# Optimization experiments

Hardware: AMD Instinct MI355X
Metric: run time of the kernel (lower is better)

Reference implementation:

```python
import jax, jax.numpy as jnp
import numpy as np

# ---------------- static model configuration (mirrors NeuroNN.__init__) -------------
N = 2000
RATIO = 0.8
N_E = int(N * RATIO)
N_I = N - N_E
NMAX = 60          # Euler fixed-point steps (Nmax in Euler2fixedpt)
NAVG = 15          # trailing steps averaged for convergence metric (Navg)
DT = 1e-3
XTOL = 1e-5
XMIN = 1.0
V_THR = 20.0       # spike threshold of Ricciardi transfer fn (V_rest = 0)
SCALING_G = 1.0
W_FF = 30.0
SIG_EXT = 5.0
DEG = jnp.pi / 180.0

_IS_I = jnp.arange(N) >= N_E
PREF = jnp.concatenate([jnp.linspace(0.0, 179.99, N_E), jnp.linspace(0.0, 179.99, N_I)])
T_INV = 1.0 / jnp.where(_IS_I, 0.01 * 0.5, 0.01)          # T_E=0.01, T_I=0.005
TAU = jnp.where(_IS_I, 0.01, 0.01)                          # tau_E = tau_I = 0.01
TAU_REF = jnp.where(_IS_I, 0.001, 0.005)                    # refractory periods
# connection-type gather index: conn[i,j] = 2*(j is I) + (i is I)  -> 0:ee 1:ei 2:ie 3:ii
CONN = 2 * _IS_I[None, :].astype(jnp.int32) + _IS_I[:, None].astype(jnp.int32)
SIGN_COL = jnp.where(_IS_I, -1.0, 1.0)                      # Dale's law: sign by presynaptic column
DIFF = jnp.abs(PREF[:, None] - PREF[None, :])               # |pref_i - pref_j| (deg)

ORIENTATIONS = jnp.arange(12.0) * 15.0                       # [12]
CONTRASTS = jnp.array([0.0, 0.0432773, 0.103411, 0.186966, 0.303066, 0.464386, 0.68854, 1.0])
# circular Gaussian feed-forward drive, [12, N]
_gauss = jnp.exp((jnp.cos(2.0 * DEG * (ORIENTATIONS[:, None] - PREF[None, :])) - 1.0)
                 / (4.0 * (DEG * W_FF) ** 2))
# all 96 conditions flattened: index c*12 + o, shape [96, N]
INPUT_MEAN = (CONTRASTS[:, None, None] * 20.0 * SCALING_G * _gauss[None]).reshape(96, N)

# ------------- Ricciardi transfer function Phi (Sanzeni rational approximation) ------
_A = [0.22757881388024176, 0.77373949685442023, 0.32056016125642045,
      0.32171431660633076, 0.62718906618071668, 0.93524391761244940,
      1.0616084849547165, 0.64290613877355551, 0.14805913578876898]

def f_ricci(x):
    t = -x / (1.0 + x)
    p = jnp.zeros_like(x)
    for c in reversed(_A):      # Horner: a1*t + ... + a9*t^9
        p = p * t + c
    return jnp.log(2.0 * x + 1.0) + p * t

def g_ricci(x):
    z = x / (2.0 + x)
    enum = (3.5441754117462949 * z - 7.0529131065835378 * z**2 - 56.532378057580381 * z**3
            + 279.56761105465944 * z**4 - 520.37554793489681 * z**5
            + 456.58245777026514 * z**6 - 155.73340457809226 * z**7)
    denom = (1.0 - 4.1357968834226053 * z - 7.2984226138266743 * z**2
             + 98.656602235468327 * z**3 - 334.20436223415163 * z**4
             + 601.08633903294185 * z**5 - 599.58577549598340 * z**6
             + 277.18420330693891 * z**7 - 16.445022798669722 * z**8)
    return enum / denom

def Phi(mu, sigma, tau, tau_ref):
    xp = mu / sigma
    xm = (mu - V_THR) / sigma
    pos = xm > 0
    neg = xp <= 0
    mid = (~pos) & (~neg)
    # branch 1: 0 < xm < xp   (guard values keep unselected lanes finite for vjp)
    xps = jnp.where(pos, xp, 2.0)
    xms = jnp.where(pos, xm, 1.0)
    r_pos = 1.0 / (f_ricci(xps) - f_ricci(xms))
    # branch 2: xm <= 0 < xp
    xpm = jnp.where(mid, xp, 1.0)
    nxm = jnp.clip(jnp.where(mid, -xm, 1.0), 0.0, 9.0)
    r_mid = 1.0 / (f_ricci(xpm) + jnp.exp(nxm ** 2) * g_ricci(nxm))
    # branch 3: xm < xp <= 0
    nxp = jnp.clip(jnp.where(neg, -xp, 0.5), 0.0, 9.0)
    nxm2 = jnp.clip(jnp.where(neg, -xm, 1.0), 0.0, 9.0)
    arg = g_ricci(nxm2) - jnp.exp(nxp ** 2 - nxm2 ** 2) * g_ricci(nxp)
    r_neg = jnp.exp(-nxm2 ** 2 - jnp.log(jnp.maximum(arg, 1e-12)))
    r = jnp.where(pos, r_pos, jnp.where(mid, r_mid, r_neg))
    return 1.0 / (tau_ref + tau / jnp.maximum(r, 1e-12))

# --------------------------- weight construction ------------------------------------
def _build_weights(j_param, p_param, w_param, rand_matrix):
    J = jnp.exp(j_param)                         # positive efficacies, [4]
    P = jax.nn.sigmoid(2.0 * jnp.exp(p_param))   # probs in (0,1), steepness-2 sigmoid
    Wd = jnp.exp(w_param)                        # positive widths (deg)
    J_mat = J[CONN]                              # [N, N] gathers by connection type
    P_mat = P[CONN]
    W_mat = Wd[CONN]
    z = jnp.exp((jnp.cos(2.0 * DEG * DIFF) - 1.0) / (4.0 * (DEG * W_mat) ** 2))
    W = SIGN_COL[None, :] * J_mat * jax.nn.sigmoid(32.0 * (P_mat * z - rand_matrix))
    return W, W * W

# ------------------ Euler fixed-point solve, all 96 conditions at once ---------------
def _solve(W, W2):
    sd2 = SIG_EXT ** 2
    def step(r, _):
        mu = TAU * (r @ W.T) + INPUT_MEAN                  # [96, N]
        sig = jnp.sqrt(TAU * (r @ W2.T) + sd2)
        dr = DT * T_INV * (Phi(mu, sig, TAU, TAU_REF) - r)
        r = r + dr
        m = jnp.max(jnp.abs(dr) / jnp.maximum(jnp.abs(r), XMIN), axis=1) / XTOL  # [96]
        return r, m
    r0 = jnp.zeros((96, N), dtype=W.dtype)
    r_fp, ms = jax.lax.scan(step, r0, None, length=NMAX)
    avg_step = jnp.mean(ms[-NAVG:])
    return r_fp, avg_step

def setup_inputs() -> dict:
    key = jax.random.key(0)
    k1, k2, k3, k4 = jax.random.split(key, 4)
    j_param = jnp.log(jnp.array([2.0, 1.5, 3.0, 2.5], dtype=jnp.float32)) + 0.1 * jax.random.normal(k1, (4,), dtype=jnp.float32)
    p_param = jnp.log(jnp.array([0.4, 0.3, 0.5, 0.4], dtype=jnp.float32)) + 0.1 * jax.random.normal(k2, (4,), dtype=jnp.float32)
    w_param = jnp.log(jnp.array([32.0, 32.0, 32.0, 32.0], dtype=jnp.float32)) + 0.1 * jax.random.normal(k3, (4,), dtype=jnp.float32)
    rand_matrix = jax.random.uniform(k4, (N, N), dtype=jnp.float32)
    return {"j_param": j_param, "p_param": p_param, "w_param": w_param, "rand_matrix": rand_matrix}

def reference(j_param, p_param, w_param, rand_matrix):
    W, W2 = _build_weights(j_param, p_param, w_param, rand_matrix)
    r_fp, avg_step = _solve(W, W2)
    # [96, N] -> [8, 12, N] -> [N, contrasts, orientations] (matches permute(2,0,1))
    tuning = r_fp.reshape(8, 12, N).transpose(2, 0, 1)
    return tuning, avg_step
```

## Files before the change

### kernel.cpp

```cpp
#include <hip/hip_runtime.h>
#include <hip/hip_bf16.h>

#define N_NEUR 2000
#define N_E    1600
#define KPAD   2048
#define NCOND  96
#define NSTEP  60
#define NAVG   15
#define NBLK   250
#define RSTEP  (NCOND * KPAD)

#define DEGF   0.017453292519943295f
#define TWO_DEG 0.03490658503988659f

typedef __attribute__((ext_vector_type(8))) short bf16x8;
typedef __attribute__((ext_vector_type(4))) float f32x4;

__device__ __forceinline__ float f_ricci(float x){
    float t = -x / (1.0f + x);
    float p = 0.14805913578876898f;
    p = fmaf(p, t, 0.64290613877355551f);
    p = fmaf(p, t, 1.0616084849547165f);
    p = fmaf(p, t, 0.93524391761244940f);
    p = fmaf(p, t, 0.62718906618071668f);
    p = fmaf(p, t, 0.32171431660633076f);
    p = fmaf(p, t, 0.32056016125642045f);
    p = fmaf(p, t, 0.77373949685442023f);
    p = fmaf(p, t, 0.22757881388024176f);
    return __logf(2.0f * x + 1.0f) + p * t;
}

__device__ __forceinline__ float g_ricci(float x){
    float z = x / (2.0f + x);
    float z2 = z * z, z3 = z2 * z, z4 = z2 * z2, z5 = z4 * z, z6 = z3 * z3, z7 = z6 * z, z8 = z4 * z4;
    float en = 3.5441754117462949f * z - 7.0529131065835378f * z2 - 56.532378057580381f * z3
             + 279.56761105465944f * z4 - 520.37554793489681f * z5
             + 456.58245777026514f * z6 - 155.73340457809226f * z7;
    float de = 1.0f - 4.1357968834226053f * z - 7.2984226138266743f * z2
             + 98.656602235468327f * z3 - 334.20436223415163f * z4
             + 601.08633903294185f * z5 - 599.58577549598340f * z6
             + 277.18420330693891f * z7 - 16.445022798669722f * z8;
    return en / de;
}

__device__ __forceinline__ float phi_rate(float mu, float sigma, float tau_ref){
    const float tau = 0.01f;
    float xp = mu / sigma;
    float xm = (mu - 20.0f) / sigma;
    float r;
    if (xm > 0.0f){
        r = 1.0f / (f_ricci(xp) - f_ricci(xm));
    } else if (xp > 0.0f){
        float nxm = fminf(-xm, 9.0f);
        r = 1.0f / (f_ricci(xp) + __expf(nxm * nxm) * g_ricci(nxm));
    } else {
        float nxp = fminf(fmaxf(-xp, 0.0f), 9.0f);
        float nxm = fminf(-xm, 9.0f);
        float arg = g_ricci(nxm) - __expf(nxp * nxp - nxm * nxm) * g_ricci(nxp);
        r = __expf(-nxm * nxm - __logf(fmaxf(arg, 1e-12f)));
    }
    return 1.0f / (tau_ref + tau / fmaxf(r, 1e-12f));
}

__device__ __forceinline__ float pref_of(int n){
    return (n < N_E) ? (float)n * (179.99f / 1599.0f)
                     : (float)(n - N_E) * (179.99f / 399.0f);
}

__device__ __forceinline__ unsigned short bf16_rne(float f){
    unsigned int u = __float_as_uint(f);
    u = (u + 0x7fffu + ((u >> 16) & 1u)) >> 16;
    return (unsigned short)u;
}

__device__ __forceinline__ void vmdrain(){
    asm volatile("s_waitcnt vmcnt(0)" ::: "memory");
}

__global__ __launch_bounds__(256) void build_w_kernel(
    const float* __restrict__ jp, const float* __restrict__ pp,
    const float* __restrict__ wp, const float* __restrict__ rnd,
    unsigned short* __restrict__ Wh, unsigned short* __restrict__ Wl,
    unsigned short* __restrict__ W2h)
{
    int e = blockIdx.x * 256 + threadIdx.x;
    int i = e >> 11;
    int j = e & (KPAD - 1);
    float w = 0.0f;
    if (i < N_NEUR && j < N_NEUR){
        int isIi = (i >= N_E) ? 1 : 0;
        int isIj = (j >= N_E) ? 1 : 0;
        int conn = 2 * isIj + isIi;
        float J  = expf(jp[conn]);
        float P  = 1.0f / (1.0f + expf(-2.0f * expf(pp[conn])));
        float Wd = expf(wp[conn]);
        float diff = fabsf(pref_of(i) - pref_of(j));
        float dw = DEGF * Wd;
        float z = expf((cosf(TWO_DEG * diff) - 1.0f) / (4.0f * dw * dw));
        float s = 1.0f / (1.0f + expf(-32.0f * (P * z - rnd[i * N_NEUR + j])));
        float sign = isIj ? -1.0f : 1.0f;
        w = sign * J * s;
    }
    unsigned short hb = bf16_rne(w);
    float hf = __uint_as_float(((unsigned int)hb) << 16);
    Wh[e] = hb;
    Wl[e] = bf16_rne(w - hf);
    W2h[e] = bf16_rne(w * w);
}

__global__ __launch_bounds__(256) void build_im_kernel(float* __restrict__ IM)
{
    int e = blockIdx.x * 256 + threadIdx.x;
    int c = e >> 11;
    int n = e & (KPAD - 1);
    if (n >= N_NEUR){ IM[e] = 0.0f; return; }
    const float contrasts[8] = {0.0f, 0.0432773f, 0.103411f, 0.186966f,
                                0.303066f, 0.464386f, 0.68854f, 1.0f};
    int ci = c / 12;
    int oi = c - ci * 12;
    float orient = (float)oi * 15.0f;
    const float dw = DEGF * 30.0f;
    float g = expf((cosf(TWO_DEG * (orient - pref_of(n))) - 1.0f) / (4.0f * dw * dw));
    IM[e] = contrasts[ci] * 20.0f * g;
}

__global__ __launch_bounds__(512, 2) void solve_kernel(
    const unsigned short* __restrict__ Wh, const unsigned short* __restrict__ Wl,
    const unsigned short* __restrict__ W2h,
    unsigned short* __restrict__ rh, unsigned short* __restrict__ rl,
    unsigned int* __restrict__ flags,
    const float* __restrict__ IM, float* __restrict__ out,
    float* __restrict__ mloc)
{
    __shared__ float red[8][64][25];
    __shared__ float vbuf[48][16];

    const int bid  = blockIdx.x;
    const int tile = bid >> 1;
    const int half = bid & 1;
    const int t  = threadIdx.x;
    const int wv = t >> 6;
    const int ln = t & 63;
    const int nbase = tile * 16;
    const int cbase = half * 48;

    const int lrow = ln & 15;
    const int lk8  = (ln >> 4) * 8;
    const int kw   = wv * 256 + lk8;
    const int nrow = nbase + lrow;

    const unsigned short* pwh = &Wh [nrow * KPAD + kw];
    const unsigned short* pwl = &Wl [nrow * KPAD + kw];
    const unsigned short* pw2 = &W2h[nrow * KPAD + kw];
    bf16x8 wh_f[8], wl_f[8], w2_f[8];
    #pragma unroll
    for (int s = 0; s < 8; ++s){
        wh_f[s] = *reinterpret_cast<const bf16x8*>(pwh + s * 32);
        wl_f[s] = *reinterpret_cast<const bf16x8*>(pwl + s * 32);
        w2_f[s] = *reinterpret_cast<const bf16x8*>(pw2 + s * 32);
    }
    #pragma unroll
    for (int s = 0; s < 8; ++s){
        asm volatile("" : "+v"(wh_f[s]));
        asm volatile("" : "+v"(wl_f[s]));
        asm volatile("" : "+v"(w2_f[s]));
    }

    const int wt = wv * 16 + (ln & 15);
    const bool need = (ln < 16) && (wt < 125);
    const unsigned int* fpoll = &flags[((size_t)wt * 2 + half) * 16];

    const int o0 = t, o1 = t + 512;
    const bool has1 = (o1 < 768);
    const int c_l0 = o0 >> 4, n_l0 = o0 & 15;
    const int c_l1 = o1 >> 4, n_l1 = o1 & 15;
    const int m0 = c_l0 >> 4, q0 = c_l0 & 3, lr0 = ((c_l0 & 15) >> 2) * 16 + n_l0;
    const int m1 = c_l1 >> 4, q1 = c_l1 & 3, lr1 = ((c_l1 & 15) >> 2) * 16 + n_l1;
    const int c0 = cbase + c_l0, i0n = nbase + n_l0;
    const int c1 = cbase + c_l1, i1n = nbase + n_l1;
    const float im0 = IM[c0 * KPAD + i0n];
    const float im1 = has1 ? IM[c1 * KPAD + i1n] : 0.0f;
    const bool isI0 = (i0n >= N_E), isI1 = (i1n >= N_E);
    float rf0 = 0.0f, rf1 = 0.0f;

    const int ro0 = (cbase + lrow) * KPAD + kw;

    for (int st = 0; st < NSTEP; ++st){
        if (st > 0){
            const unsigned int* fp = fpoll + (size_t)st * 256 * 16;
            for (;;){
                unsigned int v = need ? __hip_atomic_load(fp, __ATOMIC_RELAXED,
                                                          __HIP_MEMORY_SCOPE_AGENT) : 1u;
                if (__all(v != 0)) break;
            }
        }

        const unsigned short* bhp = rh + (size_t)st * RSTEP + ro0;
        const unsigned short* blp = rl + (size_t)st * RSTEP + ro0;

        f32x4 accm[3], accs[3];
        #pragma unroll
        for (int m = 0; m < 3; ++m){
            accm[m] = (f32x4){0.0f, 0.0f, 0.0f, 0.0f};
            accs[m] = (f32x4){0.0f, 0.0f, 0.0f, 0.0f};
        }

        bf16x8 fh[3][3], fl[3][3];
        #define LOADF(b, s) do {                                                        \
            fh[b][0] = *reinterpret_cast<const bf16x8*>(bhp + (s) * 32            );    \
            fh[b][1] = *reinterpret_cast<const bf16x8*>(bhp + (s) * 32 + 16 * KPAD);    \
            fh[b][2] = *reinterpret_cast<const bf16x8*>(bhp + (s) * 32 + 32 * KPAD);    \
            fl[b][0] = *reinterpret_cast<const bf16x8*>(blp + (s) * 32            );    \
            fl[b][1] = *reinterpret_cast<const bf16x8*>(blp + (s) * 32 + 16 * KPAD);    \
            fl[b][2] = *reinterpret_cast<const bf16x8*>(blp + (s) * 32 + 32 * KPAD);    \
        } while (0)

        LOADF(0, 0);
        LOADF(1, 1);
        #pragma unroll
        for (int s = 0; s < 8; ++s){
            const int cur = s % 3;
            if (s + 2 < 8){ const int nx = (s + 2) % 3; LOADF(nx, s + 2); }
            #pragma unroll
            for (int m = 0; m < 3; ++m){
                accm[m] = __builtin_amdgcn_mfma_f32_16x16x32_bf16(fh[cur][m], wh_f[s], accm[m], 0, 0, 0);
                accm[m] = __builtin_amdgcn_mfma_f32_16x16x32_bf16(fh[cur][m], wl_f[s], accm[m], 0, 0, 0);
                accm[m] = __builtin_amdgcn_mfma_f32_16x16x32_bf16(fl[cur][m], wh_f[s], accm[m], 0, 0, 0);
                accs[m] = __builtin_amdgcn_mfma_f32_16x16x32_bf16(fh[cur][m], w2_f[s], accs[m], 0, 0, 0);
                accs[m] = __builtin_amdgcn_mfma_f32_16x16x32_bf16(fl[cur][m], w2_f[s], accs[m], 0, 0, 0);
            }
        }
        #undef LOADF

        #pragma unroll
        for (int m = 0; m < 3; ++m)
            #pragma unroll
            for (int q = 0; q < 4; ++q){
                red[wv][ln][m * 4 + q]      = accm[m][q];
                red[wv][ln][12 + m * 4 + q] = accs[m][q];
            }
        __syncthreads();

        unsigned short* rho = rh + (size_t)(st + 1) * RSTEP;
        unsigned short* rlo = rl + (size_t)(st + 1) * RSTEP;
        const bool track = (st >= NSTEP - NAVG);

        {
            float ms = 0.0f, ss = 0.0f;
            #pragma unroll
            for (int w = 0; w < 8; ++w){
                ms += red[w][lr0][m0 * 4 + q0];
                ss += red[w][lr0][12 + m0 * 4 + q0];
            }
            const float mu = fmaf(0.01f, ms, im0);
            const float sg = sqrtf(fmaf(0.01f, ss, 25.0f));
            const float rate = phi_rate(mu, sg, isI0 ? 0.001f : 0.005f);
            const float dr = (isI0 ? 0.2f : 0.1f) * (rate - rf0);
            const float rnew = rf0 + dr;
            rf0 = rnew;
            const unsigned short hb = bf16_rne(rnew);
            const float hf = __uint_as_float(((unsigned int)hb) << 16);
            __hip_atomic_store(&rho[c0 * KPAD + i0n], hb,
                               __ATOMIC_RELAXED, __HIP_MEMORY_SCOPE_AGENT);
            __hip_atomic_store(&rlo[c0 * KPAD + i0n], bf16_rne(rnew - hf),
                               __ATOMIC_RELAXED, __HIP_MEMORY_SCOPE_AGENT);
            if (track) vbuf[c_l0][n_l0] = fabsf(dr) / fmaxf(fabsf(rnew), 1.0f);
            if (st == NSTEP - 1) out[i0n * NCOND + c0] = rnew;
        }
        if (has1){
            float ms = 0.0f, ss = 0.0f;
            #pragma unroll
            for (int w = 0; w < 8; ++w){
                ms += red[w][lr1][m1 * 4 + q1];
                ss += red[w][lr1][12 + m1 * 4 + q1];
            }
            const float mu = fmaf(0.01f, ms, im1);
            const float sg = sqrtf(fmaf(0.01f, ss, 25.0f));
            const float rate = phi_rate(mu, sg, isI1 ? 0.001f : 0.005f);
            const float dr = (isI1 ? 0.2f : 0.1f) * (rate - rf1);
            const float rnew = rf1 + dr;
            rf1 = rnew;
            const unsigned short hb = bf16_rne(rnew);
            const float hf = __uint_as_float(((unsigned int)hb) << 16);
            __hip_atomic_store(&rho[c1 * KPAD + i1n], hb,
                               __ATOMIC_RELAXED, __HIP_MEMORY_SCOPE_AGENT);
            __hip_atomic_store(&rlo[c1 * KPAD + i1n], bf16_rne(rnew - hf),
                               __ATOMIC_RELAXED, __HIP_MEMORY_SCOPE_AGENT);
            if (track) vbuf[c_l1][n_l1] = fabsf(dr) / fmaxf(fabsf(rnew), 1.0f);
            if (st == NSTEP - 1) out[i1n * NCOND + c1] = rnew;
        }

        vmdrain();
        __syncthreads();
        if (st < NSTEP - 1 && t == 0)
            __hip_atomic_store(&flags[((size_t)(st + 1) * 256 + tile * 2 + half) * 16], 1u,
                               __ATOMIC_RELAXED, __HIP_MEMORY_SCOPE_AGENT);
        if (track && t < 48){
            float mx = 0.0f;
            #pragma unroll
            for (int j = 0; j < 16; ++j) mx = fmaxf(mx, vbuf[t][j]);
            mloc[((size_t)(st - (NSTEP - NAVG)) * NBLK + bid) * 48 + t] = mx;
        }
    }
}

__global__ __launch_bounds__(128) void finalize_max_kernel(
    const float* __restrict__ mloc, float* __restrict__ m2)
{
    int idx = blockIdx.x * 128 + threadIdx.x;
    if (idx >= NAVG * NCOND) return;
    int st = idx / NCOND, c = idx - st * NCOND;
    int half = c / 48, cl = c - half * 48;
    float mx = 0.0f;
    for (int tile = 0; tile < 125; ++tile)
        mx = fmaxf(mx, mloc[((size_t)st * NBLK + tile * 2 + half) * 48 + cl]);
    m2[idx] = mx;
}

__global__ __launch_bounds__(256) void finalize_sum_kernel(
    const float* __restrict__ m2, float* __restrict__ out)
{
    __shared__ float sbuf[256];
    float s = 0.0f;
    for (int i = threadIdx.x; i < NAVG * NCOND; i += 256) s += m2[i];
    sbuf[threadIdx.x] = s;
    __syncthreads();
    for (int st = 128; st > 0; st >>= 1){
        if (threadIdx.x < st) sbuf[threadIdx.x] += sbuf[threadIdx.x + st];
        __syncthreads();
    }
    if (threadIdx.x == 0)
        out[N_NEUR * NCOND] = sbuf[0] / (float)(NAVG * NCOND) * 1e5f;
}

extern "C" void kernel_launch(void* const* d_in, const int* in_sizes, int n_in,
                              void* d_out, int out_size, void* d_ws, size_t ws_size,
                              hipStream_t stream) {
    const float* jp  = (const float*)d_in[0];
    const float* pp  = (const float*)d_in[1];
    const float* wp  = (const float*)d_in[2];
    const float* rnd = (const float*)d_in[3];
    float* out = (float*)d_out;

    const size_t WELEMS = (size_t)KPAD * KPAD;
    const size_t RBUFS  = (size_t)(NSTEP + 1) * RSTEP;
    unsigned short* Wh  = (unsigned short*)d_ws;
    unsigned short* Wl  = Wh  + WELEMS;
    unsigned short* W2h = Wl  + WELEMS;
    float* IM   = (float*)(W2h + WELEMS);
    float* mloc = IM + (size_t)NCOND * KPAD;
    float* m2   = mloc + (size_t)NAVG * NBLK * 48;
    unsigned short* rh = (unsigned short*)(m2 + NAVG * NCOND);
    unsigned short* rl = rh + RBUFS;
    unsigned int* flags = (unsigned int*)(rl + RBUFS);

    hipMemsetAsync(rh, 0, (size_t)RSTEP * sizeof(unsigned short), stream);
    hipMemsetAsync(rl, 0, (size_t)RSTEP * sizeof(unsigned short), stream);
    hipMemsetAsync(flags, 0, (size_t)(NSTEP + 1) * 256 * 16 * sizeof(unsigned int), stream);

    build_w_kernel<<<(int)(WELEMS / 256), 256, 0, stream>>>(jp, pp, wp, rnd, Wh, Wl, W2h);
    build_im_kernel<<<(int)((NCOND * KPAD) / 256), 256, 0, stream>>>(IM);

    solve_kernel<<<dim3(NBLK), dim3(512), 0, stream>>>(
        Wh, Wl, W2h, rh, rl, flags, IM, out, mloc);

    finalize_max_kernel<<<(NAVG * NCOND + 127) / 128, 128, 0, stream>>>(mloc, m2);
    finalize_sum_kernel<<<1, 256, 0, stream>>>(m2, out);
}
```

Before: 885.7 us.

## Widen neuron tile to 32 per block, halving block count and sync fan-in

Each block now covers 32 output neurons instead of 16, giving 126 blocks instead of 250. The rate fragments loaded per step are reused across two weight column groups, and each wave holds twice as many register-resident weights. The cross-wave reduction becomes a two-phase LDS add over 4 slots, and the epilogue handles three outputs per thread, masking the padded neurons past 2000. The goal is to halve the redundant global loads of the rate vector and the number of flags each step's barrier polls. The cost is higher register pressure (48 weight fragments plus 24 accumulators) and fewer blocks to spread over the CUs.

New measurement: 1.261 ms. +42.3%, slower.

```diff
diff --git a/kernel.cpp b/kernel.cpp
--- a/kernel.cpp
+++ b/kernel.cpp
@@ -7,7 +7,8 @@
 #define NCOND  96
 #define NSTEP  60
 #define NAVG   15
-#define NBLK   250
+#define NBLK   126
+#define NTILE  63
 #define RSTEP  (NCOND * KPAD)
 
 #define DEGF   0.017453292519943295f
@@ -132,8 +133,8 @@
     const float* __restrict__ IM, float* __restrict__ out,
     float* __restrict__ mloc)
 {
-    __shared__ float red[8][64][25];
-    __shared__ float vbuf[48][16];
+    __shared__ float red[4][64][49];
+    __shared__ float vbuf[48][32];
 
     const int bid  = blockIdx.x;
     const int tile = bid >> 1;
@@ -141,47 +142,53 @@
     const int t  = threadIdx.x;
     const int wv = t >> 6;
     const int ln = t & 63;
-    const int nbase = tile * 16;
+    const int nbase = tile * 32;
     const int cbase = half * 48;
 
     const int lrow = ln & 15;
     const int lk8  = (ln >> 4) * 8;
     const int kw   = wv * 256 + lk8;
-    const int nrow = nbase + lrow;
-
-    const unsigned short* pwh = &Wh [nrow * KPAD + kw];
-    const unsigned short* pwl = &Wl [nrow * KPAD + kw];
-    const unsigned short* pw2 = &W2h[nrow * KPAD + kw];
-    bf16x8 wh_f[8], wl_f[8], w2_f[8];
+
+    const int wrow0 = (nbase + lrow) * KPAD + kw;
+    const int wrow1 = (nbase + 16 + lrow) * KPAD + kw;
+    bf16x8 wh_f[8][2], wl_f[8][2], w2_f[8][2];
     #pragma unroll
     for (int s = 0; s < 8; ++s){
-        wh_f[s] = *reinterpret_cast<const bf16x8*>(pwh + s * 32);
-        wl_f[s] = *reinterpret_cast<const bf16x8*>(pwl + s * 32);
-        w2_f[s] = *reinterpret_cast<const bf16x8*>(pw2 + s * 32);
-    }
+        wh_f[s][0] = *reinterpret_cast<const bf16x8*>(Wh  + wrow0 + s * 32);
+        wh_f[s][1] = *reinterpret_cast<const bf16x8*>(Wh  + wrow1 + s * 32);
+        wl_f[s][0] = *reinterpret_cast<const bf16x8*>(Wl  + wrow0 + s * 32);
+        wl_f[s][1] = *reinterpret_cast<const bf16x8*>(Wl  + wrow1 + s * 32);
+        w2_f[s][0] = *reinterpret_cast<const bf16x8*>(W2h + wrow0 + s * 32);
+        w2_f[s][1] = *reinterpret_cast<const bf16x8*>(W2h + wrow1 + s * 32);
+    }
+
+    const int wt = wv * 8 + (ln & 7);
+    const bool need = (ln < 8) && (wt < NTILE);
+    const unsigned int* fpoll = &flags[((size_t)wt * 2 + half) * 16];
+
+    int   ep_idx[3], ep_lane[3], ep_r[3], ep_o[3];
+    float ep_im[3], ep_tref[3], ep_gain[3];
+    bool  ep_real[3];
+    float rfv[3] = {0.0f, 0.0f, 0.0f};
     #pragma unroll
-    for (int s = 0; s < 8; ++s){
-        asm volatile("" : "+v"(wh_f[s]));
-        asm volatile("" : "+v"(wl_f[s]));
-        asm volatile("" : "+v"(w2_f[s]));
-    }
-
-    const int wt = wv * 16 + (ln & 15);
-    const bool need = (ln < 16) && (wt < 125);
-    const unsigned int* fpoll = &flags[((size_t)wt * 2 + half) * 16];
-
-    const int o0 = t, o1 = t + 512;
-    const bool has1 = (o1 < 768);
-    const int c_l0 = o0 >> 4, n_l0 = o0 & 15;
-    const int c_l1 = o1 >> 4, n_l1 = o1 & 15;
-    const int m0 = c_l0 >> 4, q0 = c_l0 & 3, lr0 = ((c_l0 & 15) >> 2) * 16 + n_l0;
-    const int m1 = c_l1 >> 4, q1 = c_l1 & 3, lr1 = ((c_l1 & 15) >> 2) * 16 + n_l1;
-    const int c0 = cbase + c_l0, i0n = nbase + n_l0;
-    const int c1 = cbase + c_l1, i1n = nbase + n_l1;
-    const float im0 = IM[c0 * KPAD + i0n];
-    const float im1 = has1 ? IM[c1 * KPAD + i1n] : 0.0f;
-    const bool isI0 = (i0n >= N_E), isI1 = (i1n >= N_E);
-    float rf0 = 0.0f, rf1 = 0.0f;
+    for (int u = 0; u < 3; ++u){
+        const int o = t + u * 512;
+        const int c_l = o >> 5, n_l = o & 31;
+        const int m_e = c_l >> 4;
+        const int rr  = c_l & 15;
+        const int ng  = n_l >> 4;
+        ep_idx[u]  = (m_e * 2 + ng) * 4 + (rr & 3);
+        ep_lane[u] = (rr >> 2) * 16 + (n_l & 15);
+        const int c_g = cbase + c_l;
+        const int i_g = nbase + n_l;
+        ep_real[u] = (i_g < N_NEUR);
+        ep_r[u]    = c_g * KPAD + i_g;
+        ep_o[u]    = i_g * NCOND + c_g;
+        ep_im[u]   = ep_real[u] ? IM[c_g * KPAD + i_g] : 0.0f;
+        const bool isI = (i_g >= N_E);
+        ep_tref[u] = isI ? 0.001f : 0.005f;
+        ep_gain[u] = isI ? 0.2f : 0.1f;
+    }
 
     const int ro0 = (cbase + lrow) * KPAD + kw;
 
@@ -189,21 +196,23 @@
         if (st > 0){
             const unsigned int* fp = fpoll + (size_t)st * 256 * 16;
             for (;;){
-                unsigned int v = need ? __hip_atomic_load(fp, __ATOMIC_RELAXED,
-                                                          __HIP_MEMORY_SCOPE_AGENT) : 1u;
-                if (__all(v != 0)) break;
+                unsigned int vfl = need ? __hip_atomic_load(fp, __ATOMIC_RELAXED,
+                                                            __HIP_MEMORY_SCOPE_AGENT) : 1u;
+                if (__all(vfl != 0)) break;
             }
         }
 
         const unsigned short* bhp = rh + (size_t)st * RSTEP + ro0;
         const unsigned short* blp = rl + (size_t)st * RSTEP + ro0;
 
-        f32x4 accm[3], accs[3];
+        f32x4 accm[3][2], accs[3][2];
         #pragma unroll
-        for (int m = 0; m < 3; ++m){
-            accm[m] = (f32x4){0.0f, 0.0f, 0.0f, 0.0f};
-            accs[m] = (f32x4){0.0f, 0.0f, 0.0f, 0.0f};
-        }
+        for (int m = 0; m < 3; ++m)
+            #pragma unroll
+            for (int n = 0; n < 2; ++n){
+                accm[m][n] = (f32x4){0.0f, 0.0f, 0.0f, 0.0f};
+                accs[m][n] = (f32x4){0.0f, 0.0f, 0.0f, 0.0f};
+            }
 
         bf16x8 fh[3][3], fl[3][3];
         #define LOADF(b, s) do {                                                        \
@@ -222,72 +231,74 @@
             const int cur = s % 3;
             if (s + 2 < 8){ const int nx = (s + 2) % 3; LOADF(nx, s + 2); }
             #pragma unroll
-            for (int m = 0; m < 3; ++m){
-                accm[m] = __builtin_amdgcn_mfma_f32_16x16x32_bf16(fh[cur][m], wh_f[s], accm[m], 0, 0, 0);
-                accm[m] = __builtin_amdgcn_mfma_f32_16x16x32_bf16(fh[cur][m], wl_f[s], accm[m], 0, 0, 0);
-                accm[m] = __builtin_amdgcn_mfma_f32_16x16x32_bf16(fl[cur][m], wh_f[s], accm[m], 0, 0, 0);
-                accs[m] = __builtin_amdgcn_mfma_f32_16x16x32_bf16(fh[cur][m], w2_f[s], accs[m], 0, 0, 0);
-                accs[m] = __builtin_amdgcn_mfma_f32_16x16x32_bf16(fl[cur][m], w2_f[s], accs[m], 0, 0, 0);
-            }
+            for (int m = 0; m < 3; ++m)
+                #pragma unroll
+                for (int n = 0; n < 2; ++n){
+                    accm[m][n] = __builtin_amdgcn_mfma_f32_16x16x32_bf16(fh[cur][m], wh_f[s][n], accm[m][n], 0, 0, 0);
+                    accm[m][n] = __builtin_amdgcn_mfma_f32_16x16x32_bf16(fh[cur][m], wl_f[s][n], accm[m][n], 0, 0, 0);
+                    accm[m][n] = __builtin_amdgcn_mfma_f32_16x16x32_bf16(fl[cur][m], wh_f[s][n], accm[m][n], 0, 0, 0);
+                    accs[m][n] = __builtin_amdgcn_mfma_f32_16x16x32_bf16(fh[cur][m], w2_f[s][n], accs[m][n], 0, 0, 0);
+                    accs[m][n] = __builtin_amdgcn_mfma_f32_16x16x32_bf16(fl[cur][m], w2_f[s][n], accs[m][n], 0, 0, 0);
+                }
         }
         #undef LOADF
 
-        #pragma unroll
-        for (int m = 0; m < 3; ++m)
-            #pragma unroll
-            for (int q = 0; q < 4; ++q){
-                red[wv][ln][m * 4 + q]      = accm[m][q];
-                red[wv][ln][12 + m * 4 + q] = accs[m][q];
-            }
+        if (wv >= 4){
+            #pragma unroll
+            for (int m = 0; m < 3; ++m)
+                #pragma unroll
+                for (int n = 0; n < 2; ++n)
+                    #pragma unroll
+                    for (int q = 0; q < 4; ++q){
+                        red[wv - 4][ln][(m * 2 + n) * 4 + q]      = accm[m][n][q];
+                        red[wv - 4][ln][24 + (m * 2 + n) * 4 + q] = accs[m][n][q];
+                    }
+        }
+        __syncthreads();
+        if (wv < 4){
+            #pragma unroll
+            for (int m = 0; m < 3; ++m)
+                #pragma unroll
+                for (int n = 0; n < 2; ++n)
+                    #pragma unroll
+                    for (int q = 0; q < 4; ++q){
+                        red[wv][ln][(m * 2 + n) * 4 + q]      += accm[m][n][q];
+                        red[wv][ln][24 + (m * 2 + n) * 4 + q] += accs[m][n][q];
+                    }
+        }
         __syncthreads();
 
         unsigned short* rho = rh + (size_t)(st + 1) * RSTEP;
         unsigned short* rlo = rl + (size_t)(st + 1) * RSTEP;
         const bool track = (st >= NSTEP - NAVG);
 
-        {
+        #pragma unroll
+        for (int u = 0; u < 3; ++u){
             float ms = 0.0f, ss = 0.0f;
             #pragma unroll
-            for (int w = 0; w < 8; ++w){
-                ms += red[w][lr0][m0 * 4 + q0];
-                ss += red[w][lr0][12 + m0 * 4 + q0];
-            }
-            const float mu = fmaf(0.01f, ms, im0);
+            for (int w = 0; w < 4; ++w){
+                ms += red[w][ep_lane[u]][ep_idx[u]];
+                ss += red[w][ep_lane[u]][24 + ep_idx[u]];
+            }
+            const float mu = fmaf(0.01f, ms, ep_im[u]);
             const float sg = sqrtf(fmaf(0.01f, ss, 25.0f));
-            const float rate = phi_rate(mu, sg, isI0 ? 0.001f : 0.005f);
-            const float dr = (isI0 ? 0.2f : 0.1f) * (rate - rf0);
-            const float rnew = rf0 + dr;
-            rf0 = rnew;
-            const unsigned short hb = bf16_rne(rnew);
-            const float hf = __uint_as_float(((unsigned int)hb) << 16);
-            __hip_atomic_store(&rho[c0 * KPAD + i0n], hb,
-                               __ATOMIC_RELAXED, __HIP_MEMORY_SCOPE_AGENT);
-            __hip_atomic_store(&rlo[c0 * KPAD + i0n], bf16_rne(rnew - hf),
-                               __ATOMIC_RELAXED, __HIP_MEMORY_SCOPE_AGENT);
-            if (track) vbuf[c_l0][n_l0] = fabsf(dr) / fmaxf(fabsf(rnew), 1.0f);
-            if (st == NSTEP - 1) out[i0n * NCOND + c0] = rnew;
-        }
-        if (has1){
-            float ms = 0.0f, ss = 0.0f;
-            #pragma unroll
-            for (int w = 0; w < 8; ++w){
-                ms += red[w][lr1][m1 * 4 + q1];
-                ss += red[w][lr1][12 + m1 * 4 + q1];
-            }
-            const float mu = fmaf(0.01f, ms, im1);
-            const float sg = sqrtf(fmaf(0.01f, ss, 25.0f));
-            const float rate = phi_rate(mu, sg, isI1 ? 0.001f : 0.005f);
-            const float dr = (isI1 ? 0.2f : 0.1f) * (rate - rf1);
-            const float rnew = rf1 + dr;
-            rf1 = rnew;
-            const unsigned short hb = bf16_rne(rnew);
-            const float hf = __uint_as_float(((unsigned int)hb) << 16);
-            __hip_atomic_store(&rho[c1 * KPAD + i1n], hb,
-                               __ATOMIC_RELAXED, __HIP_MEMORY_SCOPE_AGENT);
-            __hip_atomic_store(&rlo[c1 * KPAD + i1n], bf16_rne(rnew - hf),
-                               __ATOMIC_RELAXED, __HIP_MEMORY_SCOPE_AGENT);
-            if (track) vbuf[c_l1][n_l1] = fabsf(dr) / fmaxf(fabsf(rnew), 1.0f);
-            if (st == NSTEP - 1) out[i1n * NCOND + c1] = rnew;
+            const float rate = phi_rate(mu, sg, ep_tref[u]);
+            const float dr = ep_gain[u] * (rate - rfv[u]);
+            const float rnew = rfv[u] + dr;
+            rfv[u] = rnew;
+            if (ep_real[u]){
+                const unsigned short hb = bf16_rne(rnew);
+                const float hf = __uint_as_float(((unsigned int)hb) << 16);
+                __hip_atomic_store(&rho[ep_r[u]], hb,
+                                   __ATOMIC_RELAXED, __HIP_MEMORY_SCOPE_AGENT);
+                __hip_atomic_store(&rlo[ep_r[u]], bf16_rne(rnew - hf),
+                                   __ATOMIC_RELAXED, __HIP_MEMORY_SCOPE_AGENT);
+                if (st == NSTEP - 1) out[ep_o[u]] = rnew;
+            }
+            if (track){
+                const int o = t + u * 512;
+                vbuf[o >> 5][o & 31] = ep_real[u] ? (fabsf(dr) / fmaxf(fabsf(rnew), 1.0f)) : 0.0f;
+            }
         }
 
         vmdrain();
@@ -298,7 +309,7 @@
         if (track && t < 48){
             float mx = 0.0f;
             #pragma unroll
-            for (int j = 0; j < 16; ++j) mx = fmaxf(mx, vbuf[t][j]);
+            for (int j = 0; j < 32; ++j) mx = fmaxf(mx, vbuf[t][j]);
             mloc[((size_t)(st - (NSTEP - NAVG)) * NBLK + bid) * 48 + t] = mx;
         }
     }
@@ -312,7 +323,7 @@
     int st = idx / NCOND, c = idx - st * NCOND;
     int half = c / 48, cl = c - half * 48;
     float mx = 0.0f;
-    for (int tile = 0; tile < 125; ++tile)
+    for (int tile = 0; tile < NTILE; ++tile)
         mx = fmaxf(mx, mloc[((size_t)st * NBLK + tile * 2 + half) * 48 + cl]);
     m2[idx] = mx;
 }
```
